# Kernel tuning notes

Hardware: AMD Instinct MI355X
Metric: run time of the kernel (lower is better)

Reference implementation:

```python
import jax, jax.numpy as jnp
import numpy as np

LOG_STD_MIN, LOG_STD_MAX = -20.0, 2.0

B, OBS, ACT, M, HID = 131072, 17, 6, 8, 256


def setup_inputs() -> dict:
    key = jax.random.key(0)
    ks = jax.random.split(key, 10)
    w = lambda k, *sh: (jax.random.normal(k, sh, dtype=jnp.float32) * 0.05)
    z = lambda *sh: jnp.zeros(sh, dtype=jnp.float32)
    return {
        "obs": jax.random.normal(ks[0], (B, OBS), dtype=jnp.float32),
        # encoder MLP (two tanh layers; encoder.out is unused by forward)
        "enc_W1": w(ks[1], OBS, HID), "enc_b1": z(HID),
        "enc_W2": w(ks[2], HID, HID), "enc_b2": z(HID),
        # m per-chart Gaussian heads
        "head_muW": w(ks[3], M, HID, ACT), "head_mub": z(M, ACT),
        "head_logstd": z(M, ACT),
        # value head MLP
        "val_W1": w(ks[4], HID, HID), "val_b1": z(HID),
        "val_W2": w(ks[5], HID, HID), "val_b2": z(HID),
        "val_W3": w(ks[6], HID, 1), "val_b3": z(1),
        # chart cover (pre-initialized; non-trainable in torch module)
        "centers": jax.random.normal(ks[7], (M, HID), dtype=jnp.float32),
        "stats_mean": z(HID),
        "stats_var": jnp.ones((HID,), dtype=jnp.float32),
    }


def reference(obs, enc_W1, enc_b1, enc_W2, enc_b2,
              head_muW, head_mub, head_logstd,
              val_W1, val_b1, val_W2, val_b2, val_W3, val_b3,
              centers, stats_mean, stats_var):
    # shared encoder phi(o): two tanh layers -> feat [B, HID]
    h = jnp.tanh(obs @ enc_W1 + enc_b1)
    feat = jnp.tanh(h @ enc_W2 + enc_b2)

    # hard Voronoi chart routing on detached, whitened features
    zf = jax.lax.stop_gradient(feat)
    zw = (zf - stats_mean) * jax.lax.rsqrt(stats_var + 1e-6)
    # squared distances to centers: [B, M] (argmin of d^2 == argmin of d)
    d2 = (jnp.sum(zw * zw, axis=-1, keepdims=True)
          - 2.0 * (zw @ centers.T)
          + jnp.sum(centers * centers, axis=-1))
    hard_idx = jnp.argmin(d2, axis=1)  # [B]

    # per-chart Gaussian heads, then gather the selected head per sample
    mu_all = jnp.einsum('bd,mda->bma', feat, head_muW) + head_mub  # [B, M, ACT]
    mu = jnp.take_along_axis(mu_all, hard_idx[:, None, None], axis=1)[:, 0, :]
    log_std = jnp.clip(head_logstd[hard_idx], LOG_STD_MIN, LOG_STD_MAX)  # [B, ACT]

    # value head V(feat)
    v1 = jnp.tanh(feat @ val_W1 + val_b1)
    v2 = jnp.tanh(v1 @ val_W2 + val_b2)
    v = (v2 @ val_W3 + val_b3)[:, 0]  # [B]

    # policy params (post-clamp, as stored in SquashedDiagGaussian) + value
    return jnp.concatenate([mu, log_std, v[:, None]], axis=-1)  # [B, 2*ACT+1]
```

## Files before the change

kernel.cpp:

```cpp
#include <hip/hip_runtime.h>
#include <math.h>

typedef __attribute__((ext_vector_type(8))) short bf16x8;
typedef __attribute__((ext_vector_type(4))) float f32x4;

#define B_TOT 131072
#define NOBS 17
#define NACT 6
#define NM 8
#define HID 256
#define TS 64
#define NT 512
#define NW 8
#define NOUT 13
#define EPS_MARGIN 0.20f
#define CAPF 65536

#define AST 264
#define OST 40
#define MUST 52
#define SCST 12

#define OFF_FLAGS 64
#define OFF_W1H  (OFF_FLAGS + 4*CAPF)
#define OFF_W1L  (OFF_W1H + 256*32*2)
#define OFF_W2T  (OFF_W1L + 256*32*2)
#define OFF_V1T  (OFF_W2T + 256*256*2)
#define OFF_V2T  (OFF_V1T + 256*256*2)
#define OFF_HDT  (OFF_V2T + 256*256*2)
#define OFF_G0   (OFF_HDT + 64*256*2)
#define WS_NEED  (OFF_G0 + 64)

__device__ __forceinline__ unsigned short f2bf(float f) {
  unsigned int u = __float_as_uint(f);
  u = (u + 0x7fffu + ((u >> 16) & 1u)) >> 16;
  return (unsigned short)u;
}
__device__ __forceinline__ float bf2f(unsigned short h) {
  return __uint_as_float(((unsigned int)h) << 16);
}
__device__ __forceinline__ float tanh_fast2(float x) {
  float e = __expf(2.0f * x);
  float r = __builtin_amdgcn_rcpf(e + 1.0f);
  return 1.0f - 2.0f * r;
}
__device__ __forceinline__ unsigned int pk2(float a, float b) {
  unsigned int r;
  asm("v_cvt_pk_bf16_f32 %0, %1, %2" : "=v"(r) : "v"(a), "v"(b));
  return r;
}
__device__ __forceinline__ f32x4 MFMA(bf16x8 a, bf16x8 b, f32x4 c) {
  return __builtin_amdgcn_mfma_f32_16x16x32_bf16(a, b, c, 0, 0, 0);
}

extern "C" __global__ void ppo_zero(int* cnt) {
  if (cnt && threadIdx.x == 0) cnt[0] = 0;
}

extern "C" __global__ __launch_bounds__(256)
void ppo_prep(const float* __restrict__ eW1, const float* __restrict__ eW2,
              const float* __restrict__ vW1, const float* __restrict__ vW2,
              const float* __restrict__ muW, const float* __restrict__ cen,
              const float* __restrict__ svar, unsigned char* wsb)
{
  int t = blockIdx.x * 256 + threadIdx.x;
  if (t < 65536) {
    int c = t >> 8, k = t & 255;
    ((unsigned short*)(wsb + OFF_W2T))[c * 256 + k] = f2bf(eW2[k * 256 + c]);
  } else if (t < 131072) {
    int u = t - 65536; int c = u >> 8, k = u & 255;
    ((unsigned short*)(wsb + OFF_V1T))[c * 256 + k] = f2bf(vW1[k * 256 + c]);
  } else if (t < 196608) {
    int u = t - 131072; int c = u >> 8, k = u & 255;
    ((unsigned short*)(wsb + OFF_V2T))[c * 256 + k] = f2bf(vW2[k * 256 + c]);
  } else if (t < 212992) {
    int u = t - 196608; int c = u >> 8, k = u & 255;
    float v = 0.f;
    if (c < 48) { int m = c / 6, a = c - 6 * m; v = muW[(m * 256 + k) * 6 + a]; }
    else if (c < 56) {
      int m = c - 48;
      double s = 1.0 / sqrt((double)svar[k] + 1e-6);
      v = (float)(-2.0 * s * (double)cen[m * 256 + k]);
    }
    ((unsigned short*)(wsb + OFF_HDT))[c * 256 + k] = f2bf(v);
  } else if (t < 221184) {
    int u = t - 212992; int c = u >> 5, k = u & 31;
    float v = (k < NOBS) ? eW1[k * 256 + c] : 0.f;
    unsigned short hi = f2bf(v);
    ((unsigned short*)(wsb + OFF_W1H))[c * 32 + k] = hi;
    ((unsigned short*)(wsb + OFF_W1L))[c * 32 + k] = f2bf(v - bf2f(hi));
  }
}

extern "C" __global__ __launch_bounds__(NT)
void ppo_prep_g0(const float* __restrict__ cen, const float* __restrict__ smean,
                 const float* __restrict__ svar, unsigned char* wsb)
{
  int m = threadIdx.x >> 6, lane = threadIdx.x & 63;
  double acc = 0.0;
  for (int k = lane; k < HID; k += 64) {
    double s = 1.0 / sqrt((double)svar[k] + 1e-6);
    double c = (double)cen[m * HID + k];
    acc += c * (2.0 * (double)smean[k] * s + c);
  }
#pragma unroll
  for (int w = 32; w >= 1; w >>= 1) acc += __shfl_xor(acc, w);
  if (lane == 0) ((float*)(wsb + OFF_G0))[m] = (float)acc;
}

template<int CT>
__device__ __forceinline__ void gemm256(const unsigned short* __restrict__ WT,
                                        const unsigned short* act,
                                        int cb, int l15, int h, f32x4 acc[CT][4])
{
#pragma unroll
  for (int kt = 0; kt < 8; ++kt) {
    int kk = kt * 32 + 8 * h;
    bf16x8 a[CT], b[4];
#pragma unroll
    for (int ct = 0; ct < CT; ++ct)
      a[ct] = *(const bf16x8*)(WT + (cb + 16 * ct + l15) * 256 + kk);
#pragma unroll
    for (int nt = 0; nt < 4; ++nt)
      b[nt] = *(const bf16x8*)(act + (16 * nt + l15) * AST + kk);
#pragma unroll
    for (int ct = 0; ct < CT; ++ct)
#pragma unroll
      for (int nt = 0; nt < 4; ++nt)
        acc[ct][nt] = MFMA(a[ct], b[nt], acc[ct][nt]);
  }
}

__device__ __forceinline__ void epi_tanh_store(f32x4 acc[2][4], unsigned short* dst,
                                               int cb, int l15, int h)
{
#pragma unroll
  for (int ct = 0; ct < 2; ++ct)
#pragma unroll
    for (int nt = 0; nt < 4; ++nt) {
      float t0 = tanh_fast2(acc[ct][nt][0]);
      float t1 = tanh_fast2(acc[ct][nt][1]);
      float t2 = tanh_fast2(acc[ct][nt][2]);
      float t3 = tanh_fast2(acc[ct][nt][3]);
      uint2 u; u.x = pk2(t0, t1); u.y = pk2(t2, t3);
      *(uint2*)(dst + (16 * nt + l15) * AST + cb + 16 * ct + 4 * h) = u;
    }
}

extern "C" __global__ __launch_bounds__(NT, 4)
void ppo_mfma(const float* __restrict__ obs,
              const float* __restrict__ eb1, const float* __restrict__ eb2,
              const float* __restrict__ mub, const float* __restrict__ logstd,
              const float* __restrict__ vb1, const float* __restrict__ vb2,
              const float* __restrict__ vW3, const float* __restrict__ vb3,
              const unsigned char* __restrict__ wsb,
              float* __restrict__ out, int* cnt, int* flags, int cap)
{
  __shared__ unsigned short Hb[TS * AST];
  __shared__ unsigned short Fb[TS * AST];
  __shared__ unsigned short MU[TS * MUST];
  __shared__ float SC[TS * SCST];
  __shared__ float VP[NW * TS];
  __shared__ float LS[48];

  const int tid = threadIdx.x, lane = tid & 63, wid = tid >> 6;
  const int l15 = lane & 15, h = lane >> 4;
  const int cb = wid * 32;
  const int s0 = blockIdx.x * TS;

  const unsigned short* W1H = (const unsigned short*)(wsb + OFF_W1H);
  const unsigned short* W1L = (const unsigned short*)(wsb + OFF_W1L);
  const unsigned short* W2T = (const unsigned short*)(wsb + OFF_W2T);
  const unsigned short* V1T = (const unsigned short*)(wsb + OFF_V1T);
  const unsigned short* V2T = (const unsigned short*)(wsb + OFF_V2T);
  const unsigned short* HDT = (const unsigned short*)(wsb + OFF_HDT);
  const float* g0g = (const float*)(wsb + OFF_G0);

  unsigned short* OBH = Fb;
  unsigned short* OBL = Fb + TS * OST;

  for (int t = tid; t < TS * NOBS; t += NT) {
    int s = t / NOBS, k = t - NOBS * s;
    float v = obs[(size_t)s0 * NOBS + t];
    unsigned short hi = f2bf(v);
    OBH[s * OST + k] = hi;
    OBL[s * OST + k] = f2bf(v - bf2f(hi));
  }
  for (int t = tid; t < TS * (32 - NOBS); t += NT) {
    int s = t / (32 - NOBS), k = NOBS + t - (32 - NOBS) * s;
    OBH[s * OST + k] = 0; OBL[s * OST + k] = 0;
  }
  if (tid < 48) LS[tid] = fminf(fmaxf(logstd[tid], -20.f), 2.f);
  __syncthreads();

  {
    f32x4 acc[2][4];
    f32x4 b0 = *(const f32x4*)(eb1 + cb + 4 * h);
    f32x4 b1 = *(const f32x4*)(eb1 + cb + 16 + 4 * h);
#pragma unroll
    for (int nt = 0; nt < 4; ++nt) { acc[0][nt] = b0; acc[1][nt] = b1; }
    bf16x8 aH[2], aL[2], bH[4], bL[4];
#pragma unroll
    for (int ct = 0; ct < 2; ++ct) {
      aH[ct] = *(const bf16x8*)(W1H + (cb + 16 * ct + l15) * 32 + 8 * h);
      aL[ct] = *(const bf16x8*)(W1L + (cb + 16 * ct + l15) * 32 + 8 * h);
    }
#pragma unroll
    for (int nt = 0; nt < 4; ++nt) {
      bH[nt] = *(const bf16x8*)(OBH + (16 * nt + l15) * OST + 8 * h);
      bL[nt] = *(const bf16x8*)(OBL + (16 * nt + l15) * OST + 8 * h);
    }
#pragma unroll
    for (int ct = 0; ct < 2; ++ct)
#pragma unroll
      for (int nt = 0; nt < 4; ++nt) {
        acc[ct][nt] = MFMA(aH[ct], bH[nt], acc[ct][nt]);
        acc[ct][nt] = MFMA(aL[ct], bH[nt], acc[ct][nt]);
        acc[ct][nt] = MFMA(aH[ct], bL[nt], acc[ct][nt]);
      }
    epi_tanh_store(acc, Hb, cb, l15, h);
  }
  __syncthreads();

  {
    f32x4 acc[2][4];
    f32x4 b0 = *(const f32x4*)(eb2 + cb + 4 * h);
    f32x4 b1 = *(const f32x4*)(eb2 + cb + 16 + 4 * h);
#pragma unroll
    for (int nt = 0; nt < 4; ++nt) { acc[0][nt] = b0; acc[1][nt] = b1; }
    gemm256<2>(W2T, Hb, cb, l15, h, acc);
    epi_tanh_store(acc, Fb, cb, l15, h);
  }
  __syncthreads();

  {
    f32x4 acc[2][4];
    f32x4 b0 = *(const f32x4*)(vb1 + cb + 4 * h);
    f32x4 b1 = *(const f32x4*)(vb1 + cb + 16 + 4 * h);
#pragma unroll
    for (int nt = 0; nt < 4; ++nt) { acc[0][nt] = b0; acc[1][nt] = b1; }
    gemm256<2>(V1T, Fb, cb, l15, h, acc);
    epi_tanh_store(acc, Hb, cb, l15, h);
  }
  if (wid < 4) {
    f32x4 hacc[1][4];
    f32x4 hb;
    if (wid < 3)      hb = *(const f32x4*)(mub + 16 * wid + 4 * h);
    else if (h < 2)   hb = *(const f32x4*)(g0g + 4 * h);
    else              hb = (f32x4){0.f, 0.f, 0.f, 0.f};
#pragma unroll
    for (int nt = 0; nt < 4; ++nt) hacc[0][nt] = hb;
    gemm256<1>(HDT, Fb, 16 * wid, l15, h, hacc);
    if (wid < 3) {
#pragma unroll
      for (int nt = 0; nt < 4; ++nt) {
        uint2 u;
        u.x = pk2(hacc[0][nt][0], hacc[0][nt][1]);
        u.y = pk2(hacc[0][nt][2], hacc[0][nt][3]);
        *(uint2*)(MU + (16 * nt + l15) * MUST + 16 * wid + 4 * h) = u;
      }
    } else if (h < 2) {
#pragma unroll
      for (int nt = 0; nt < 4; ++nt)
        *(f32x4*)(SC + (16 * nt + l15) * SCST + 4 * h) = hacc[0][nt];
    }
  }
  __syncthreads();

  {
    f32x4 acc[2][4];
    f32x4 b0 = *(const f32x4*)(vb2 + cb + 4 * h);
    f32x4 b1 = *(const f32x4*)(vb2 + cb + 16 + 4 * h);
#pragma unroll
    for (int nt = 0; nt < 4; ++nt) { acc[0][nt] = b0; acc[1][nt] = b1; }
    gemm256<2>(V2T, Hb, cb, l15, h, acc);
    f32x4 w30 = *(const f32x4*)(vW3 + cb + 4 * h);
    f32x4 w31 = *(const f32x4*)(vW3 + cb + 16 + 4 * h);
#pragma unroll
    for (int nt = 0; nt < 4; ++nt) {
      float v = 0.f;
#pragma unroll
      for (int r = 0; r < 4; ++r) {
        v = fmaf(tanh_fast2(acc[0][nt][r]), w30[r], v);
        v = fmaf(tanh_fast2(acc[1][nt][r]), w31[r], v);
      }
      v += __shfl_xor(v, 16);
      v += __shfl_xor(v, 32);
      if (h == 0) VP[wid * TS + 16 * nt + l15] = v;
    }
  }
  __syncthreads();

  if (wid == 0) {
    int s = lane;
    int best = 0;
    float bs = SC[s * SCST], bs2 = 3.4e38f;
#pragma unroll
    for (int m = 1; m < NM; ++m) {
      float sm = SC[s * SCST + m];
      if (sm < bs) { bs2 = bs; bs = sm; best = m; }
      else if (sm < bs2) bs2 = sm;
    }
    if (cnt && (bs2 - bs) < EPS_MARGIN) {
      int idx = atomicAdd(cnt, 1);
      if (idx < cap) flags[idx] = s0 + s;
    }
    float v = vb3[0];
#pragma unroll
    for (int w = 0; w < NW; ++w) v += VP[w * TS + s];
    float* orow = out + (size_t)(s0 + s) * NOUT;
#pragma unroll
    for (int a = 0; a < NACT; ++a) orow[a] = bf2f(MU[s * MUST + best * NACT + a]);
#pragma unroll
    for (int a = 0; a < NACT; ++a) orow[NACT + a] = LS[best * NACT + a];
    orow[2 * NACT] = v;
  }
}

extern "C" __global__ __launch_bounds__(256, 2)
void ppo_recheck(const float* __restrict__ obs,
                 const float* __restrict__ eW1, const float* __restrict__ eb1,
                 const float* __restrict__ eW2, const float* __restrict__ eb2,
                 const float* __restrict__ muW, const float* __restrict__ mub,
                 const float* __restrict__ logstd,
                 const float* __restrict__ cen, const float* __restrict__ smean,
                 const float* __restrict__ svar,
                 float* __restrict__ out,
                 const int* cnt, const int* flags, int cap)
{
  if (!cnt) return;
  __shared__ double hbuf[HID];
  __shared__ double fbuf[HID];
  __shared__ double d2buf[NM];
  __shared__ double obsd[NOBS];
  __shared__ int bestv;
  const int tid = threadIdx.x;
  const int n = min(cnt[0], cap);

  for (int i = blockIdx.x; i < n; i += gridDim.x) {
    const int s = flags[i];
    if (tid < NOBS) obsd[tid] = (double)obs[(size_t)s * NOBS + tid];
    __syncthreads();
    double a1 = (double)eb1[tid];
    for (int k = 0; k < NOBS; ++k) a1 = fma(obsd[k], (double)eW1[k * HID + tid], a1);
    hbuf[tid] = tanh(a1);
    __syncthreads();
    double a2 = (double)eb2[tid];
    for (int k = 0; k < HID; ++k) a2 = fma(hbuf[k], (double)eW2[k * HID + tid], a2);
    fbuf[tid] = tanh(a2);
    __syncthreads();
    {
      int g = tid >> 5, l = tid & 31;
      double dot = 0.0, zn = 0.0, cn = 0.0;
      for (int j = 0; j < HID / 32; ++j) {
        int k = l + j * 32;
        double zs = 1.0 / sqrt((double)svar[k] + 1e-6);
        double zw = (fbuf[k] - (double)smean[k]) * zs;
        double ck = (double)cen[g * HID + k];
        dot = fma(zw, ck, dot);
        zn  = fma(zw, zw, zn);
        cn  = fma(ck, ck, cn);
      }
      for (int m = 16; m >= 1; m >>= 1) {
        dot += __shfl_xor(dot, m, 32);
        zn  += __shfl_xor(zn,  m, 32);
        cn  += __shfl_xor(cn,  m, 32);
      }
      if (l == 0) d2buf[g] = zn - 2.0 * dot + cn;
    }
    __syncthreads();
    if (tid == 0) {
      int best = 0;
      double bs = d2buf[0];
      for (int m = 1; m < NM; ++m)
        if (d2buf[m] < bs) { bs = d2buf[m]; best = m; }
      bestv = best;
    }
    __syncthreads();
    const int best = bestv;
    if (tid < NACT) {
      float acc = mub[best * NACT + tid];
      for (int k = 0; k < HID; ++k)
        acc = fmaf((float)fbuf[k], muW[(best * HID + k) * NACT + tid], acc);
      out[(size_t)s * NOUT + tid] = acc;
    } else if (tid < 2 * NACT) {
      int a = tid - NACT;
      float ls = logstd[best * NACT + a];
      out[(size_t)s * NOUT + NACT + a] = fminf(fmaxf(ls, -20.0f), 2.0f);
    }
    __syncthreads();
  }
}

extern "C" __global__ __launch_bounds__(NT, 4)
void ppo_fp32_fb(const float* __restrict__ obs,
                 const float* __restrict__ eW1, const float* __restrict__ eb1,
                 const float* __restrict__ eW2, const float* __restrict__ eb2,
                 const float* __restrict__ muW, const float* __restrict__ mub,
                 const float* __restrict__ logstd,
                 const float* __restrict__ vW1, const float* __restrict__ vb1,
                 const float* __restrict__ vW2, const float* __restrict__ vb2,
                 const float* __restrict__ vW3, const float* __restrict__ vb3,
                 const float* __restrict__ cen, const float* __restrict__ smean,
                 const float* __restrict__ svar,
                 float* __restrict__ out, int* cnt, int* flags, int cap)
{
  __shared__ float act[HID * TS];
  __shared__ float mubuf[NM * TS * NACT];
  __shared__ float scbuf[NM * TS];
  __shared__ float zsbuf[HID];
  const int tid  = threadIdx.x;
  const int lane = tid & 63;
  const int wid  = tid >> 6;
  const int c0   = wid * 32;
  const int s0   = blockIdx.x * TS;
  float* obs_s = mubuf;
  for (int idx = tid; idx < TS * NOBS; idx += NT) {
    int s = idx / NOBS, i = idx - s * NOBS;
    obs_s[i * TS + s] = obs[s0 * NOBS + idx];
  }
  if (tid < HID) zsbuf[tid] = (float)(1.0 / sqrt((double)svar[tid] + 1e-6));
  __syncthreads();
  {
    float acc[32];
#pragma unroll
    for (int c = 0; c < 32; ++c) acc[c] = eb1[c0 + c];
    float ob[NOBS];
#pragma unroll
    for (int i = 0; i < NOBS; ++i) ob[i] = obs_s[i * TS + lane];
#pragma unroll
    for (int i = 0; i < NOBS; ++i) {
      const float* w = &eW1[i * HID + c0];
#pragma unroll
      for (int c = 0; c < 32; ++c) acc[c] = fmaf(ob[i], w[c], acc[c]);
    }
#pragma unroll
    for (int c = 0; c < 32; ++c) act[(c0 + c) * TS + lane] = tanh_fast2(acc[c]);
  }
  __syncthreads();
  {
    float acc[32];
#pragma unroll
    for (int c = 0; c < 32; ++c) acc[c] = eb2[c0 + c];
#pragma unroll 4
    for (int k = 0; k < HID; ++k) {
      float a = act[k * TS + lane];
      const float* w = &eW2[k * HID + c0];
#pragma unroll
      for (int c = 0; c < 32; ++c) acc[c] = fmaf(a, w[c], acc[c]);
    }
    __syncthreads();
#pragma unroll
    for (int c = 0; c < 32; ++c) act[(c0 + c) * TS + lane] = tanh_fast2(acc[c]);
  }
  __syncthreads();
  {
    double dot = 0.0, zn = 0.0, cn = 0.0;
    float mu[NACT];
#pragma unroll
    for (int a = 0; a < NACT; ++a) mu[a] = mub[wid * NACT + a];
#pragma unroll 2
    for (int k = 0; k < HID; ++k) {
      float f = act[k * TS + lane];
      double zw = ((double)f - (double)smean[k]) * (double)zsbuf[k];
      double ck = (double)cen[wid * HID + k];
      dot = fma(zw, ck, dot); zn = fma(zw, zw, zn); cn = fma(ck, ck, cn);
      const float* w = &muW[(wid * HID + k) * NACT];
#pragma unroll
      for (int a = 0; a < NACT; ++a) mu[a] = fmaf(f, w[a], mu[a]);
    }
    scbuf[wid * TS + lane] = (float)(zn - 2.0 * dot + cn);
#pragma unroll
    for (int a = 0; a < NACT; ++a) mubuf[(wid * TS + lane) * NACT + a] = mu[a];
  }
  {
    float acc[32];
#pragma unroll
    for (int c = 0; c < 32; ++c) acc[c] = vb1[c0 + c];
#pragma unroll 4
    for (int k = 0; k < HID; ++k) {
      float f = act[k * TS + lane];
      const float* w = &vW1[k * HID + c0];
#pragma unroll
      for (int c = 0; c < 32; ++c) acc[c] = fmaf(f, w[c], acc[c]);
    }
    __syncthreads();
#pragma unroll
    for (int c = 0; c < 32; ++c) act[(c0 + c) * TS + lane] = tanh_fast2(acc[c]);
  }
  __syncthreads();
  {
    float acc[32];
#pragma unroll
    for (int c = 0; c < 32; ++c) acc[c] = vb2[c0 + c];
#pragma unroll 4
    for (int k = 0; k < HID; ++k) {
      float f = act[k * TS + lane];
      const float* w = &vW2[k * HID + c0];
#pragma unroll
      for (int c = 0; c < 32; ++c) acc[c] = fmaf(f, w[c], acc[c]);
    }
    __syncthreads();
#pragma unroll
    for (int c = 0; c < 32; ++c) act[(c0 + c) * TS + lane] = tanh_fast2(acc[c]);
  }
  __syncthreads();
  if (wid == 0) {
    int best = 0;
    float bs = scbuf[lane], bs2 = 3.4e38f;
#pragma unroll
    for (int m = 1; m < NM; ++m) {
      float sm = scbuf[m * TS + lane];
      if (sm < bs) { bs2 = bs; bs = sm; best = m; }
      else if (sm < bs2) bs2 = sm;
    }
    if (cnt && (bs2 - bs) < 1e-2f) {
      int idx = atomicAdd(cnt, 1);
      if (idx < cap) flags[idx] = s0 + lane;
    }
    float v = vb3[0];
#pragma unroll 4
    for (int k = 0; k < HID; ++k) v = fmaf(act[k * TS + lane], vW3[k], v);
    float* orow = &out[(size_t)(s0 + lane) * NOUT];
#pragma unroll
    for (int a = 0; a < NACT; ++a) orow[a] = mubuf[(best * TS + lane) * NACT + a];
#pragma unroll
    for (int a = 0; a < NACT; ++a) {
      float ls = logstd[best * NACT + a];
      orow[NACT + a] = fminf(fmaxf(ls, -20.0f), 2.0f);
    }
    orow[2 * NACT] = v;
  }
}

extern "C" void kernel_launch(void* const* d_in, const int* in_sizes, int n_in,
                              void* d_out, int out_size, void* d_ws, size_t ws_size,
                              hipStream_t stream) {
  const float* obs   = (const float*)d_in[0];
  const float* eW1   = (const float*)d_in[1];
  const float* eb1   = (const float*)d_in[2];
  const float* eW2   = (const float*)d_in[3];
  const float* eb2   = (const float*)d_in[4];
  const float* muW   = (const float*)d_in[5];
  const float* mub   = (const float*)d_in[6];
  const float* lstd  = (const float*)d_in[7];
  const float* vW1   = (const float*)d_in[8];
  const float* vb1   = (const float*)d_in[9];
  const float* vW2   = (const float*)d_in[10];
  const float* vb2   = (const float*)d_in[11];
  const float* vW3   = (const float*)d_in[12];
  const float* vb3   = (const float*)d_in[13];
  const float* cen   = (const float*)d_in[14];
  const float* smean = (const float*)d_in[15];
  const float* svar  = (const float*)d_in[16];
  float* out = (float*)d_out;
  unsigned char* wsb = (unsigned char*)d_ws;

  if (ws_size >= (size_t)WS_NEED) {
    int* cnt = (int*)wsb;
    int* flags = (int*)(wsb + OFF_FLAGS);
    hipLaunchKernelGGL(ppo_zero, dim3(1), dim3(64), 0, stream, cnt);
    hipLaunchKernelGGL(ppo_prep, dim3(864), dim3(256), 0, stream,
                       eW1, eW2, vW1, vW2, muW, cen, svar, wsb);
    hipLaunchKernelGGL(ppo_prep_g0, dim3(1), dim3(NT), 0, stream, cen, smean, svar, wsb);
    hipLaunchKernelGGL(ppo_mfma, dim3(B_TOT / TS), dim3(NT), 0, stream,
                       obs, eb1, eb2, mub, lstd, vb1, vb2, vW3, vb3,
                       (const unsigned char*)wsb, out, cnt, flags, CAPF);
    hipLaunchKernelGGL(ppo_recheck, dim3(2048), dim3(256), 0, stream,
                       obs, eW1, eb1, eW2, eb2, muW, mub, lstd,
                       cen, smean, svar, out, cnt, flags, CAPF);
  } else {
    int* cnt = nullptr; int* flags = nullptr; int cap = 0;
    if (ws_size >= 1024) {
      cnt = (int*)wsb;
      flags = cnt + 16;
      size_t c = (ws_size - 64) / 4;
      cap = (int)(c < (size_t)CAPF ? c : (size_t)CAPF);
    }
    hipLaunchKernelGGL(ppo_zero, dim3(1), dim3(64), 0, stream, cnt);
    hipLaunchKernelGGL(ppo_fp32_fb, dim3(B_TOT / TS), dim3(NT), 0, stream,
                       obs, eW1, eb1, eW2, eb2, muW, mub, lstd,
                       vW1, vb1, vW2, vb2, vW3, vb3, cen, smean, svar, out,
                       cnt, flags, cap);
    hipLaunchKernelGGL(ppo_recheck, dim3(2048), dim3(256), 0, stream,
                       obs, eW1, eb1, eW2, eb2, muW, mub, lstd,
                       cen, smean, svar, out, cnt, flags, cap);
  }
}
```

Baseline: 219.9 us.

## Share one LDS activation buffer to raise occupancy and fold prep launches

Replaces the two ping-pong activation buffers with a single in-place buffer plus a reused scratch region, adding a barrier between each GEMM's reads and its epilogue writes. This cuts shared memory per block so more blocks can fit per CU, and launch bounds are raised from 4 to 6 accordingly. It also reorders the value layer-1 GEMM to after the head GEMM, since both read the features from the same buffer. Separately, the counter-zero and g0 kernels are merged into an extra prep block to save launches, and the recheck dot product is split into four accumulators. The risks are the extra barriers and register pressure from the tighter launch bound.

```diff
diff --git a/kernel.cpp b/kernel.cpp
--- a/kernel.cpp
+++ b/kernel.cpp
@@ -61,8 +61,23 @@
 void ppo_prep(const float* __restrict__ eW1, const float* __restrict__ eW2,
               const float* __restrict__ vW1, const float* __restrict__ vW2,
               const float* __restrict__ muW, const float* __restrict__ cen,
-              const float* __restrict__ svar, unsigned char* wsb)
+              const float* __restrict__ smean, const float* __restrict__ svar,
+              unsigned char* wsb, int* cnt)
 {
+  if (blockIdx.x == 864) {
+    int m = threadIdx.x >> 5, l = threadIdx.x & 31;
+    double acc = 0.0;
+    for (int k = l; k < HID; k += 32) {
+      double s = 1.0 / sqrt((double)svar[k] + 1e-6);
+      double c = (double)cen[m * HID + k];
+      acc += c * (2.0 * (double)smean[k] * s + c);
+    }
+#pragma unroll
+    for (int w = 16; w >= 1; w >>= 1) acc += __shfl_xor(acc, w, 32);
+    if (l == 0) ((float*)(wsb + OFF_G0))[m] = (float)acc;
+    if (threadIdx.x == 0) cnt[0] = 0;
+    return;
+  }
   int t = blockIdx.x * 256 + threadIdx.x;
   if (t < 65536) {
     int c = t >> 8, k = t & 255;
@@ -92,22 +107,6 @@
   }
 }
 
-extern "C" __global__ __launch_bounds__(NT)
-void ppo_prep_g0(const float* __restrict__ cen, const float* __restrict__ smean,
-                 const float* __restrict__ svar, unsigned char* wsb)
-{
-  int m = threadIdx.x >> 6, lane = threadIdx.x & 63;
-  double acc = 0.0;
-  for (int k = lane; k < HID; k += 64) {
-    double s = 1.0 / sqrt((double)svar[k] + 1e-6);
-    double c = (double)cen[m * HID + k];
-    acc += c * (2.0 * (double)smean[k] * s + c);
-  }
-#pragma unroll
-  for (int w = 32; w >= 1; w >>= 1) acc += __shfl_xor(acc, w);
-  if (lane == 0) ((float*)(wsb + OFF_G0))[m] = (float)acc;
-}
-
 template<int CT>
 __device__ __forceinline__ void gemm256(const unsigned short* __restrict__ WT,
                                         const unsigned short* act,
@@ -147,7 +146,7 @@
     }
 }
 
-extern "C" __global__ __launch_bounds__(NT, 4)
+extern "C" __global__ __launch_bounds__(NT, 6)
 void ppo_mfma(const float* __restrict__ obs,
               const float* __restrict__ eb1, const float* __restrict__ eb2,
               const float* __restrict__ mub, const float* __restrict__ logstd,
@@ -156,10 +155,8 @@
               const unsigned char* __restrict__ wsb,
               float* __restrict__ out, int* cnt, int* flags, int cap)
 {
-  __shared__ unsigned short Hb[TS * AST];
-  __shared__ unsigned short Fb[TS * AST];
-  __shared__ unsigned short MU[TS * MUST];
-  __shared__ float SC[TS * SCST];
+  __shared__ unsigned short ACT[TS * AST];
+  __shared__ uint4 SCR4[640];
   __shared__ float VP[NW * TS];
   __shared__ float LS[48];
 
@@ -176,8 +173,10 @@
   const unsigned short* HDT = (const unsigned short*)(wsb + OFF_HDT);
   const float* g0g = (const float*)(wsb + OFF_G0);
 
-  unsigned short* OBH = Fb;
-  unsigned short* OBL = Fb + TS * OST;
+  unsigned short* OBH = (unsigned short*)SCR4;
+  unsigned short* OBL = OBH + TS * OST;
+  unsigned short* MU  = (unsigned short*)SCR4;
+  float*          SC  = (float*)((char*)SCR4 + TS * MUST * 2);
 
   for (int t = tid; t < TS * NOBS; t += NT) {
     int s = t / NOBS, k = t - NOBS * s;
@@ -218,7 +217,7 @@
         acc[ct][nt] = MFMA(aL[ct], bH[nt], acc[ct][nt]);
         acc[ct][nt] = MFMA(aH[ct], bL[nt], acc[ct][nt]);
       }
-    epi_tanh_store(acc, Hb, cb, l15, h);
+    epi_tanh_store(acc, ACT, cb, l15, h);
   }
   __syncthreads();
 
@@ -228,20 +227,12 @@
     f32x4 b1 = *(const f32x4*)(eb2 + cb + 16 + 4 * h);
 #pragma unroll
     for (int nt = 0; nt < 4; ++nt) { acc[0][nt] = b0; acc[1][nt] = b1; }
-    gemm256<2>(W2T, Hb, cb, l15, h, acc);
-    epi_tanh_store(acc, Fb, cb, l15, h);
-  }
-  __syncthreads();
-
-  {
-    f32x4 acc[2][4];
-    f32x4 b0 = *(const f32x4*)(vb1 + cb + 4 * h);
-    f32x4 b1 = *(const f32x4*)(vb1 + cb + 16 + 4 * h);
-#pragma unroll
-    for (int nt = 0; nt < 4; ++nt) { acc[0][nt] = b0; acc[1][nt] = b1; }
-    gemm256<2>(V1T, Fb, cb, l15, h, acc);
-    epi_tanh_store(acc, Hb, cb, l15, h);
-  }
+    gemm256<2>(W2T, ACT, cb, l15, h, acc);
+    __syncthreads();
+    epi_tanh_store(acc, ACT, cb, l15, h);
+  }
+  __syncthreads();
+
   if (wid < 4) {
     f32x4 hacc[1][4];
     f32x4 hb;
@@ -250,7 +241,7 @@
     else              hb = (f32x4){0.f, 0.f, 0.f, 0.f};
 #pragma unroll
     for (int nt = 0; nt < 4; ++nt) hacc[0][nt] = hb;
-    gemm256<1>(HDT, Fb, 16 * wid, l15, h, hacc);
+    gemm256<1>(HDT, ACT, 16 * wid, l15, h, hacc);
     if (wid < 3) {
 #pragma unroll
       for (int nt = 0; nt < 4; ++nt) {
@@ -265,6 +256,16 @@
         *(f32x4*)(SC + (16 * nt + l15) * SCST + 4 * h) = hacc[0][nt];
     }
   }
+  {
+    f32x4 acc[2][4];
+    f32x4 b0 = *(const f32x4*)(vb1 + cb + 4 * h);
+    f32x4 b1 = *(const f32x4*)(vb1 + cb + 16 + 4 * h);
+#pragma unroll
+    for (int nt = 0; nt < 4; ++nt) { acc[0][nt] = b0; acc[1][nt] = b1; }
+    gemm256<2>(V1T, ACT, cb, l15, h, acc);
+    __syncthreads();
+    epi_tanh_store(acc, ACT, cb, l15, h);
+  }
   __syncthreads();
 
   {
@@ -273,7 +274,7 @@
     f32x4 b1 = *(const f32x4*)(vb2 + cb + 16 + 4 * h);
 #pragma unroll
     for (int nt = 0; nt < 4; ++nt) { acc[0][nt] = b0; acc[1][nt] = b1; }
-    gemm256<2>(V2T, Hb, cb, l15, h, acc);
+    gemm256<2>(V2T, ACT, cb, l15, h, acc);
     f32x4 w30 = *(const f32x4*)(vW3 + cb + 4 * h);
     f32x4 w31 = *(const f32x4*)(vW3 + cb + 16 + 4 * h);
 #pragma unroll
@@ -345,9 +346,16 @@
     for (int k = 0; k < NOBS; ++k) a1 = fma(obsd[k], (double)eW1[k * HID + tid], a1);
     hbuf[tid] = tanh(a1);
     __syncthreads();
-    double a2 = (double)eb2[tid];
-    for (int k = 0; k < HID; ++k) a2 = fma(hbuf[k], (double)eW2[k * HID + tid], a2);
-    fbuf[tid] = tanh(a2);
+    {
+      double p0 = 0.0, p1 = 0.0, p2 = 0.0, p3 = 0.0;
+      for (int k = 0; k < HID; k += 4) {
+        p0 = fma(hbuf[k],     (double)eW2[(k)     * HID + tid], p0);
+        p1 = fma(hbuf[k + 1], (double)eW2[(k + 1) * HID + tid], p1);
+        p2 = fma(hbuf[k + 2], (double)eW2[(k + 2) * HID + tid], p2);
+        p3 = fma(hbuf[k + 3], (double)eW2[(k + 3) * HID + tid], p3);
+      }
+      fbuf[tid] = tanh((double)eb2[tid] + ((p0 + p1) + (p2 + p3)));
+    }
     __syncthreads();
     {
       int g = tid >> 5, l = tid & 31;
@@ -559,10 +567,8 @@
   if (ws_size >= (size_t)WS_NEED) {
     int* cnt = (int*)wsb;
     int* flags = (int*)(wsb + OFF_FLAGS);
-    hipLaunchKernelGGL(ppo_zero, dim3(1), dim3(64), 0, stream, cnt);
-    hipLaunchKernelGGL(ppo_prep, dim3(864), dim3(256), 0, stream,
-                       eW1, eW2, vW1, vW2, muW, cen, svar, wsb);
-    hipLaunchKernelGGL(ppo_prep_g0, dim3(1), dim3(NT), 0, stream, cen, smean, svar, wsb);
+    hipLaunchKernelGGL(ppo_prep, dim3(865), dim3(256), 0, stream,
+                       eW1, eW2, vW1, vW2, muW, cen, smean, svar, wsb, cnt);
     hipLaunchKernelGGL(ppo_mfma, dim3(B_TOT / TS), dim3(NT), 0, stream,
                        obs, eb1, eb2, mub, lstd, vb1, vb2, vW3, vb3,
                        (const unsigned char*)wsb, out, cnt, flags, CAPF);
```

After: 435.7 us. 1.98x slower.
